# Performance work log

Hardware: AMD Instinct MI355X
Metric: run time of the kernel (lower is better)

Reference implementation:

```python
import jax, jax.numpy as jnp
import numpy as np

T = 16          # video_length
HEADS = 8
DIM_HEAD = 64
INNER = HEADS * DIM_HEAD   # 512
SCALE = DIM_HEAD ** -0.5
QDIM = 320      # input_dims[0]
NTOK = 1024     # num_tokens[0] == N == M (pose tokens)
CTOK = 256      # context_tokens == per-frame context tokens (16x16)
HC = WC = 16    # sqrt(CTOK)
HM = WM = 32    # after bilinear x2 upsample (sqrt(NTOK))
CDIM = 1024     # context_dim
NBLOCKS = 2
FF_INNER = 4 * QDIM  # 1280, GEGLU proj -> 2*FF_INNER


def _ln(x, w, b):
    mu = jnp.mean(x, axis=-1, keepdims=True)
    var = jnp.mean(jnp.square(x - mu), axis=-1, keepdims=True)
    return (x - mu) * jax.lax.rsqrt(var + 1e-5) * w + b


def setup_inputs() -> dict:
    key = jax.random.key(0)
    ks = jax.random.split(key, 24)
    rn = lambda i, shape, s: jax.random.normal(ks[i], shape, jnp.float32) * s
    return {
        "hidden_state": rn(0, (2 * T, NTOK, HEADS, QDIM // HEADS), 1.0),
        "context": rn(1, (2, 2, CTOK, CDIM), 1.0),
        "pose": rn(2, (2, QDIM, T, HM, WM), 1.0),
        "Wq": rn(3, (NBLOCKS, QDIM, INNER), 0.02),
        "Wk": rn(4, (NBLOCKS, CDIM, INNER), 0.02),
        "Wv": rn(5, (NBLOCKS, CDIM, INNER), 0.02),
        "Wa": rn(6, (NBLOCKS, QDIM, INNER), 0.02),
        "agent_bias": rn(7, (NBLOCKS, NTOK, CTOK), 0.01),
        "query_bias": rn(8, (NBLOCKS, NTOK, NTOK), 0.01),
        "dwc_w": rn(9, (NBLOCKS, INNER, 1, 3, 3), 0.1),
        "dwc_b": rn(10, (NBLOCKS, INNER), 0.01),
        "Wo": rn(11, (NBLOCKS, INNER, QDIM), 0.02),
        "norm_w": jnp.ones((QDIM,), jnp.float32),
        "norm_b": jnp.zeros((QDIM,), jnp.float32),
        "ffln_w": jnp.ones((QDIM,), jnp.float32),
        "ffln_b": jnp.zeros((QDIM,), jnp.float32),
        "ff_w1": rn(12, (QDIM, 2 * FF_INNER), 0.02),
        "ff_b1": jnp.zeros((2 * FF_INNER,), jnp.float32),
        "ff_w2": rn(13, (FF_INNER, QDIM), 0.02),
        "ff_b2": jnp.zeros((QDIM,), jnp.float32),
    }


def reference(hidden_state, context, pose, Wq, Wk, Wv, Wa, agent_bias, query_bias,
              dwc_w, dwc_b, Wo, norm_w, norm_b, ffln_w, ffln_b, ff_w1, ff_b1, ff_w2, ff_b2):
    B = hidden_state.shape[0] // T
    C = context.shape[1]
    # '(B T) N H D -> B T N (H D)'
    hs = hidden_state.reshape(B, T, NTOK, QDIM)
    # pose 'B D T H W -> B T (H W) D'
    pose_t = jnp.transpose(pose, (0, 2, 3, 4, 1)).reshape(B, T, NTOK, QDIM)

    for b in range(NBLOCKS):
        # ---- compute_kv_attention ----
        k = jnp.einsum('bcnd,de->bcne', context, Wk[b])          # [B,C,Nc,INNER]
        v = jnp.einsum('bcnd,de->bcne', context, Wv[b])          # [B,C,Nc,INNER]
        a_tok = jnp.einsum('btmd,de->btme', pose_t, Wa[b])       # [B,T,M,INNER]
        kf = k.reshape(B, C * CTOK, INNER)                       # 'B C N D -> B (C N) D'
        attn = jnp.einsum('btme,bne->btmn', a_tok * SCALE, kf)   # [B,T,M,C*Nc]
        # faithful to torch: view(B,T,M,N,C) then 'B T M N C -> (B C) T M N'
        attn = attn.reshape(B, T, NTOK, CTOK, C).transpose(0, 4, 1, 2, 3)  # [B,C,T,M,Nc]
        attn = jax.nn.softmax(attn + agent_bias[b], axis=-1)
        akv = jnp.einsum('bctmn,bcne->bctme', attn, v)           # [B,C,T,M,INNER]
        agent_kv = jnp.max(akv, axis=1)                          # [B,T,M,INNER]

        # depthwise conv over context-frame value maps (T-independent since v repeated over T)
        v_img = v.transpose(0, 1, 3, 2).reshape(B * C, INNER, HC, WC)
        vd = jax.lax.conv_general_dilated(
            v_img, dwc_w[b], (1, 1), 'SAME', feature_group_count=INNER,
            dimension_numbers=('NCHW', 'OIHW', 'NCHW')) + dwc_b[b][None, :, None, None]
        vd = vd.reshape(B, C, INNER, HC, WC).max(axis=1)         # max over frames
        vd = jax.image.resize(vd, (B, INNER, HM, WM), method='bilinear')  # x2, align_corners=False
        v_tok = vd.reshape(B, INNER, NTOK).transpose(0, 2, 1)[:, None]    # [B,1,N,INNER]

        # ---- agent-token cross attention ----
        nh = _ln(hs, norm_w, norm_b)
        q = jnp.einsum('btnd,de->btne', nh, Wq[b])
        aq = jax.nn.softmax(
            jnp.einsum('btne,btme->btnm', q * SCALE, a_tok) + query_bias[b], axis=-1)
        x = jnp.einsum('btnm,btme->btne', aq, agent_kv) + v_tok
        hs = jnp.einsum('btne,ed->btnd', x, Wo[b]) + hs          # residual

    # ---- LayerNorm + GEGLU FeedForward + residual ----
    h = _ln(hs, ffln_w, ffln_b)
    p = h @ ff_w1 + ff_b1
    a, g = jnp.split(p, 2, axis=-1)
    hs = (a * jax.nn.gelu(g, approximate=False)) @ ff_w2 + ff_b2 + hs
    return hs.reshape(B * T, NTOK, QDIM)
```

## Files before the change

kernel.cpp:

```cpp
#include <hip/hip_runtime.h>
#include <hip/hip_bf16.h>
#include <math.h>

typedef __hip_bfloat16 bf16;
typedef short short8 __attribute__((ext_vector_type(8)));
typedef float floatx4 __attribute__((ext_vector_type(4)));

static const int B2   = 2;
static const int TT   = 16;
static const int NTK  = 1024;
static const int CTK  = 256;
static const int QD   = 320;
static const int INNR = 512;
static const int CD   = 1024;
#define SCALE_ 0.125f

__device__ __forceinline__ ushort f2bu(float x){
  bf16 h = __float2bfloat16(x);
  return *reinterpret_cast<ushort*>(&h);
}


template<int NV>
struct StBf {
  const ushort* src; int ld; int tid;
  short8 r[NV];
  __device__ __forceinline__ void load(int k0){
#pragma unroll
    for(int v=0;v<NV;v++){
      int idx=tid+v*256, rr=idx>>2, kq=idx&3;
      r[v] = *(const short8*)&src[(size_t)rr*ld + k0 + kq*8];
    }
  }
  __device__ __forceinline__ void store(ushort* dst){
#pragma unroll
    for(int v=0;v<NV;v++){
      int idx=tid+v*256, rr=idx>>2, kq=idx&3;
      *(short8*)&dst[rr*32 + ((kq+(rr>>1))&3)*8] = r[v];
    }
  }
};

struct StT128 {
  const float* src; int ld; int tid;
  float4 r[4];
  __device__ __forceinline__ void load(int k0){
#pragma unroll
    for(int i=0;i<4;i++){
      int f4=tid+i*256, rr=f4>>3, kq=f4&7;
      r[i] = *(const float4*)(src + (size_t)rr*ld + k0 + kq*4);
    }
  }
  __device__ __forceinline__ void store(ushort* dst){
#pragma unroll
    for(int i=0;i<4;i++){
      int f4=tid+i*256, rr=f4>>3, kq=f4&7;
      int s=((kq>>1)+(rr>>1))&3;
      float4 v=r[i];
      ushort4 u={f2bu(v.x),f2bu(v.y),f2bu(v.z),f2bu(v.w)};
      *(ushort4*)&dst[rr*32 + s*8 + (kq&1)*4]=u;
    }
  }
};

struct StAtok {
  const float* base; int tid;
  float r[16];
  __device__ __forceinline__ void load(int k0){
#pragma unroll
    for(int i=0;i<16;i++){
      int e=tid+i*256, m=e&127, kk=e>>7;
      r[i]=base[(size_t)(k0+kk)*(TT*NTK) + m];
    }
  }
  __device__ __forceinline__ void store(ushort* dst){
#pragma unroll
    for(int i=0;i<16;i++){
      int e=tid+i*256, m=e&127, kk=e>>7;
      int s=((kk>>3)+(m>>1))&3;
      dst[m*32 + s*8 + (kk&7)]=f2bu(r[i]);
    }
  }
};

template<int NT>
__device__ __forceinline__ void mfma_tiles(const ushort* As, const ushort* Bs,
    floatx4 (&acc)[4][NT], int mOff, int nOff, int lane15, int quad){
  short8 af[4], bfm[NT];
  #pragma unroll
  for(int i=0;i<4;i++){
    int ar = mOff + i*16 + lane15;
    af[i] = *(const short8*)&As[ar*32 + ((quad + (ar>>1))&3)*8];
  }
  #pragma unroll
  for(int j=0;j<NT;j++){
    int br = nOff + j*16 + lane15;
    bfm[j] = *(const short8*)&Bs[br*32 + ((quad + (br>>1))&3)*8];
  }
  #pragma unroll
  for(int i=0;i<4;i++)
    #pragma unroll
    for(int j=0;j<NT;j++)
      acc[i][j] = __builtin_amdgcn_mfma_f32_16x16x32_bf16(af[i], bfm[j], acc[i][j], 0, 0, 0);
}

template<int NT>
__device__ __forceinline__ void zero_acc(floatx4 (&acc)[4][NT]){
  floatx4 z = {0.f,0.f,0.f,0.f};
  #pragma unroll
  for(int i=0;i<4;i++)
    #pragma unroll
    for(int j=0;j<NT;j++) acc[i][j]=z;
}

template<int NT, class SA, class SB>
__device__ __forceinline__ void core_db(SA& sa, SB& sb, int K,
    ushort* As0, ushort* As1, ushort* Bs0, ushort* Bs1,
    floatx4 (&acc)[4][NT], int mOff, int nOff, int lane15, int quad){
  sa.load(0); sb.load(0);
  sa.store(As0); sb.store(Bs0);
  const int nk = K>>5;
  for(int i=0;i<nk-1;i++){
    sa.load((i+1)<<5); sb.load((i+1)<<5);
    __syncthreads();
    mfma_tiles<NT>((i&1)?As1:As0, (i&1)?Bs1:Bs0, acc, mOff,nOff,lane15,quad);
    sa.store((i&1)?As0:As1); sb.store((i&1)?Bs0:Bs1);
  }
  __syncthreads();
  mfma_tiles<NT>(((nk-1)&1)?As1:As0, ((nk-1)&1)?Bs1:Bs0, acc, mOff,nOff,lane15,quad);
}

#define GEMM_IDS(NT_) \
  const int tid=threadIdx.x, w=tid>>6, lane15=tid&15, quad=(tid>>4)&3; \
  const int mOff=(w&1)*64, nOff=(w>>1)*(NT_*16);
#define EPI(NT_) \
  _Pragma("unroll") for(int i=0;i<4;i++) \
  _Pragma("unroll") for(int j=0;j<NT_;j++) \
  _Pragma("unroll") for(int r=0;r<4;r++)
#define ROWG (mOff + i*16 + quad*4 + r)
#define COLG (nOff + j*16 + lane15)

__global__ void __launch_bounds__(256) k_wtrans(const float* __restrict__ W, ushort* __restrict__ WT,
                                                int K, int N){
  __shared__ float t[64][65];
  const int kB = blockIdx.y*64, nB = blockIdx.x*64;
  for(int e=threadIdx.x; e<4096; e+=256){
    int r=e>>6, c=e&63;
    t[r][c] = W[(size_t)(kB+r)*N + nB+c];
  }
  __syncthreads();
  for(int e=threadIdx.x; e<4096; e+=256){
    int r=e>>6, c=e&63;
    WT[(size_t)(nB+r)*K + kB+c] = f2bu(t[c][r]);
  }
}

__global__ void k_ln(const float* __restrict__ hs, const float* __restrict__ w,
                     const float* __restrict__ b, ushort* __restrict__ out, int row0){
  const int r = blockIdx.x, lane = threadIdx.x;
  const float* hr = hs + (size_t)(row0+r)*QD;
  float s=0.f, s2=0.f;
  #pragma unroll
  for(int j=0;j<5;j++){ float v=hr[j*64+lane]; s+=v; s2+=v*v; }
  #pragma unroll
  for(int o=32;o;o>>=1){ s+=__shfl_down(s,o); s2+=__shfl_down(s2,o); }
  s = __shfl(s,0); s2 = __shfl(s2,0);
  float mu=s*(1.f/320.f);
  float var=s2*(1.f/320.f)-mu*mu;
  float rs=rsqrtf(var+1e-5f);
  #pragma unroll
  for(int j=0;j<5;j++){
    int c=j*64+lane;
    out[(size_t)r*QD + c] = f2bu((hr[c]-mu)*rs*w[c]+b[c]);
  }
}

__global__ void __launch_bounds__(256) g_kv(const float* __restrict__ A,
                                            const ushort* __restrict__ wkT, const ushort* __restrict__ wvT,
                                            ushort* __restrict__ kbf, float* __restrict__ vb,
                                            ushort* __restrict__ vbT){
  __shared__ ushort As[2][128*32], Bs[2][128*32];
  GEMM_IDS(4)
  const int z=blockIdx.z, b=z>>1, isv=z&1;
  const ushort* BT = (isv ? wvT : wkT) + (size_t)b*524288;
  const int rB=blockIdx.y*128, cB=blockIdx.x*128;
  floatx4 acc[4][4]; zero_acc<4>(acc);
  StT128 sa{A + (size_t)rB*CD, CD, tid};
  StBf<2> sb{BT + (size_t)cB*CD, CD, tid};
  core_db<4>(sa, sb, CD, As[0],As[1],Bs[0],Bs[1], acc, mOff,nOff,lane15,quad);
  if(!isv){
    ushort* kb = kbf + (size_t)b*524288;
    EPI(4){ kb[(size_t)(rB+ROWG)*INNR + cB+COLG] = f2bu(acc[i][j][r]); }
  }else{
    float* vf = vb + (size_t)b*524288;
    ushort* vT = vbT + (size_t)b*524288;
    EPI(4){
      int row=rB+ROWG, col=cB+COLG;
      float v=acc[i][j][r];
      vf[(size_t)row*INNR + col] = v;
      vT[((size_t)(row>>8)*INNR + col)*CTK + (row&255)] = f2bu(v);
    }
  }
}

__global__ void __launch_bounds__(256) g_atok(const float* __restrict__ pose, const ushort* __restrict__ WaT,
                                              ushort* __restrict__ atok, int pt0){
  __shared__ ushort As[2][128*32], Bs[2][128*32];
  GEMM_IDS(4)
  const int z=blockIdx.z, pt=pt0+z, bb=pt>>4, t=pt&15;
  const int rB=blockIdx.y*128, cB=blockIdx.x*128;
  floatx4 acc[4][4]; zero_acc<4>(acc);
  StAtok sa{pose + ((size_t)(bb*QD)*TT + t)*NTK + rB, tid};
  StBf<2> sb{WaT + (size_t)cB*QD, QD, tid};
  core_db<4>(sa, sb, QD, As[0],As[1],Bs[0],Bs[1], acc, mOff,nOff,lane15,quad);
  EPI(4){ atok[((size_t)z*NTK + rB+ROWG)*INNR + cB+COLG] = f2bu(acc[i][j][r]); }
}

__global__ void __launch_bounds__(256) g_logits(const ushort* __restrict__ atok, const ushort* __restrict__ kbf,
                                                const float* __restrict__ abias, float* __restrict__ lgC, int pt0){
  __shared__ ushort As[2][128*32], Bs[2][128*32];
  GEMM_IDS(4)
  const int z=blockIdx.z, zp=z>>1, c=z&1, pt=pt0+zp, bb=pt>>4;
  const int rB=blockIdx.y*128, cB=blockIdx.x*128;
  floatx4 acc[4][4]; zero_acc<4>(acc);
  StBf<2> sa{atok + ((size_t)zp*NTK + rB)*INNR, INNR, tid};
  StBf<2> sb{kbf + (size_t)(bb*512 + 2*cB + c)*INNR, 2*INNR, tid};
  core_db<4>(sa, sb, INNR, As[0],As[1],Bs[0],Bs[1], acc, mOff,nOff,lane15,quad);
  float* Cz = lgC + (size_t)(zp*2+c)*NTK*CTK;
  EPI(4){
    int row=rB+ROWG, col=cB+COLG;
    Cz[(size_t)row*CTK + col] = acc[i][j][r]*SCALE_ + abias[(size_t)row*CTK + col];
  }
}

__global__ void __launch_bounds__(256) g_pvmax(const ushort* __restrict__ lg_us, const ushort* __restrict__ vT,
                                               ushort* __restrict__ akvT, int pt0){
  __shared__ ushort As[2][128*32], Bs[2][128*32];
  GEMM_IDS(4)
  const int zp=blockIdx.z, pt=pt0+zp, bb=pt>>4;
  const int rB=blockIdx.y*128, cB=blockIdx.x*128;
  floatx4 best[4][4]; zero_acc<4>(best);
  floatx4 acc[4][4];
  for(int c=0;c<2;c++){
    if(c) __syncthreads();
    zero_acc<4>(acc);
    StBf<2> sa{lg_us + ((size_t)(zp*2+c)*NTK + rB)*INNR, INNR, tid};
    StBf<2> sb{vT + ((size_t)(bb*2+c)*INNR + cB)*CTK, CTK, tid};
    core_db<4>(sa, sb, CTK, As[0],As[1],Bs[0],Bs[1], acc, mOff,nOff,lane15,quad);
    if(c==0){
      #pragma unroll
      for(int i=0;i<4;i++)
        #pragma unroll
        for(int j=0;j<4;j++) best[i][j]=acc[i][j];
    }else{
      EPI(4){ best[i][j][r] = fmaxf(best[i][j][r], acc[i][j][r]); }
    }
  }
  #pragma unroll
  for(int i=0;i<4;i++)
    #pragma unroll
    for(int j=0;j<4;j++){
      int col = cB + nOff + j*16 + lane15;
      int row0 = rB + mOff + i*16 + quad*4;
      ushort4 u = { f2bu(best[i][j][0]), f2bu(best[i][j][1]), f2bu(best[i][j][2]), f2bu(best[i][j][3]) };
      *(ushort4*)&akvT[((size_t)zp*INNR + col)*NTK + row0] = u;
    }
}

__global__ void __launch_bounds__(256) g_q(const ushort* __restrict__ lnh, const ushort* __restrict__ WqT,
                                           ushort* __restrict__ qb){
  __shared__ ushort As[2][128*32], Bs[2][128*32];
  GEMM_IDS(4)
  const int rB=blockIdx.y*128, cB=blockIdx.x*128;
  floatx4 acc[4][4]; zero_acc<4>(acc);
  StBf<2> sa{lnh + (size_t)rB*QD, QD, tid};
  StBf<2> sb{WqT + (size_t)cB*QD, QD, tid};
  core_db<4>(sa, sb, QD, As[0],As[1],Bs[0],Bs[1], acc, mOff,nOff,lane15,quad);
  EPI(4){ qb[(size_t)(rB+ROWG)*INNR + cB+COLG] = f2bu(acc[i][j][r]); }
}

__global__ void __launch_bounds__(256) g_aql(const ushort* __restrict__ qb, const ushort* __restrict__ atok,
                                             const float* __restrict__ qbias, float* __restrict__ D){
  __shared__ ushort As[2][128*32], Bs[2][128*32];
  GEMM_IDS(4)
  const int z=blockIdx.z;
  const int rB=blockIdx.y*128, cB=blockIdx.x*128;
  floatx4 acc[4][4]; zero_acc<4>(acc);
  StBf<2> sa{qb + ((size_t)z*NTK + rB)*INNR, INNR, tid};
  StBf<2> sb{atok + ((size_t)z*NTK + cB)*INNR, INNR, tid};
  core_db<4>(sa, sb, INNR, As[0],As[1],Bs[0],Bs[1], acc, mOff,nOff,lane15,quad);
  float* Dz = D + (size_t)z*NTK*NTK;
  EPI(4){
    int row=rB+ROWG, col=cB+COLG;
    Dz[(size_t)row*NTK + col] = acc[i][j][r]*SCALE_ + qbias[(size_t)row*NTK + col];
  }
}

__global__ void __launch_bounds__(256) g_aqpv(const float* __restrict__ D, const ushort* __restrict__ akvT,
                                              const float* __restrict__ vt, ushort* __restrict__ xb, int pt0){
  __shared__ ushort As[2][128*32], Bs[2][128*32];
  GEMM_IDS(4)
  const int z=blockIdx.z, pt=pt0+z, bb=pt>>4;
  const int rB=blockIdx.y*128, cB=blockIdx.x*128;
  floatx4 acc[4][4]; zero_acc<4>(acc);
  StBf<2> sa{(const ushort*)D + (size_t)z*2097152 + (size_t)rB*2048, 2048, tid};
  StBf<2> sb{akvT + ((size_t)z*INNR + cB)*NTK, NTK, tid};
  core_db<4>(sa, sb, NTK, As[0],As[1],Bs[0],Bs[1], acc, mOff,nOff,lane15,quad);
  EPI(4){
    int row=rB+ROWG, col=cB+COLG;
    xb[((size_t)z*NTK + row)*INNR + col] = f2bu(acc[i][j][r] + vt[((size_t)bb*NTK + row)*INNR + col]);
  }
}

__global__ void __launch_bounds__(256) g_wo(const ushort* __restrict__ xb, const ushort* __restrict__ WoT,
                                            float* __restrict__ hs, int row0){
  __shared__ ushort As[2][128*32], Bs[2][64*32];
  GEMM_IDS(2)
  const int rB=blockIdx.y*128, cB=blockIdx.x*64;
  floatx4 acc[4][2]; zero_acc<2>(acc);
  StBf<2> sa{xb + (size_t)rB*INNR, INNR, tid};
  StBf<1> sb{WoT + (size_t)cB*INNR, INNR, tid};
  core_db<2>(sa, sb, INNR, As[0],As[1],Bs[0],Bs[1], acc, mOff,nOff,lane15,quad);
  EPI(2){
    size_t o = (size_t)(row0+rB+ROWG)*QD + cB+COLG;
    hs[o] = hs[o] + acc[i][j][r];
  }
}

__global__ void __launch_bounds__(256) g_ff1(const ushort* __restrict__ lnh, const ushort* __restrict__ W1T,
    const float* __restrict__ b1, ushort* __restrict__ G){
  __shared__ ushort As[2][128*32], Ba[2][64*32], Bg[2][64*32];
  GEMM_IDS(2)
  const int rB=blockIdx.y*128, cB=blockIdx.x*64;
  floatx4 accA[4][2], accG[4][2]; zero_acc<2>(accA); zero_acc<2>(accG);
  StBf<2> sa{lnh + (size_t)rB*QD, QD, tid};
  StBf<1> s1{W1T + (size_t)cB*QD, QD, tid};
  StBf<1> s2{W1T + (size_t)(1280+cB)*QD, QD, tid};
  sa.load(0); s1.load(0); s2.load(0);
  sa.store(As[0]); s1.store(Ba[0]); s2.store(Bg[0]);
  const int nk = QD>>5;
  for(int i=0;i<nk-1;i++){
    int k=(i+1)<<5;
    sa.load(k); s1.load(k); s2.load(k);
    __syncthreads();
    const int cur=i&1;
    mfma_tiles<2>(As[cur],Ba[cur],accA,mOff,nOff,lane15,quad);
    mfma_tiles<2>(As[cur],Bg[cur],accG,mOff,nOff,lane15,quad);
    sa.store(As[cur^1]); s1.store(Ba[cur^1]); s2.store(Bg[cur^1]);
  }
  __syncthreads();
  {
    const int cur=(nk-1)&1;
    mfma_tiles<2>(As[cur],Ba[cur],accA,mOff,nOff,lane15,quad);
    mfma_tiles<2>(As[cur],Bg[cur],accG,mOff,nOff,lane15,quad);
  }
  EPI(2){
    int n = cB+COLG;
    float a = accA[i][j][r] + b1[n];
    float g = accG[i][j][r] + b1[1280+n];
    G[(size_t)(rB+ROWG)*1280 + n] = f2bu(a*0.5f*g*(1.0f+erff(g*0.70710678f)));
  }
}

__global__ void __launch_bounds__(256) g_ff2(const ushort* __restrict__ G, const ushort* __restrict__ W2T,
    const float* __restrict__ b2v, float* __restrict__ hs, int row0){
  __shared__ ushort As[2][128*32], Bs[2][64*32];
  GEMM_IDS(2)
  const int rB=blockIdx.y*128, cB=blockIdx.x*64;
  floatx4 acc[4][2]; zero_acc<2>(acc);
  StBf<2> sa{G + (size_t)rB*1280, 1280, tid};
  StBf<1> sb{W2T + (size_t)cB*1280, 1280, tid};
  core_db<2>(sa, sb, 1280, As[0],As[1],Bs[0],Bs[1], acc, mOff,nOff,lane15,quad);
  EPI(2){
    int col = cB+COLG;
    size_t o = (size_t)(row0+rB+ROWG)*QD + col;
    hs[o] = acc[i][j][r] + b2v[col] + hs[o];
  }
}

__global__ void k_softmax256(float* __restrict__ buf){
  __shared__ float red[8];
  const int tid=threadIdx.x;
  size_t row=blockIdx.x;
  float x = buf[row*256+tid];
  float m = x;
  #pragma unroll
  for(int o=32;o;o>>=1) m=fmaxf(m,__shfl_down(m,o));
  if((tid&63)==0) red[tid>>6]=m;
  __syncthreads();
  if(tid==0) red[4]=fmaxf(fmaxf(red[0],red[1]),fmaxf(red[2],red[3]));
  __syncthreads();
  float M=red[4];
  float e=__expf(x-M);
  float s=e;
  #pragma unroll
  for(int o=32;o;o>>=1) s+=__shfl_down(s,o);
  if((tid&63)==0) red[tid>>6]=s;
  __syncthreads();
  if(tid==0) red[5]=red[0]+red[1]+red[2]+red[3];
  __syncthreads();
  ((ushort*)buf)[row*512 + tid] = f2bu(e/red[5]);
}

__global__ void k_softmax1024(float* __restrict__ buf){
  __shared__ float red[8];
  const int tid=threadIdx.x;
  size_t row=blockIdx.x;
  float4* p = (float4*)(buf + row*1024);
  float4 v = p[tid];
  float m = fmaxf(fmaxf(v.x,v.y),fmaxf(v.z,v.w));
  #pragma unroll
  for(int o=32;o;o>>=1) m=fmaxf(m,__shfl_down(m,o));
  if((tid&63)==0) red[tid>>6]=m;
  __syncthreads();
  if(tid==0) red[4]=fmaxf(fmaxf(red[0],red[1]),fmaxf(red[2],red[3]));
  __syncthreads();
  float M=red[4];
  v.x=__expf(v.x-M); v.y=__expf(v.y-M); v.z=__expf(v.z-M); v.w=__expf(v.w-M);
  float s=v.x+v.y+v.z+v.w;
  #pragma unroll
  for(int o=32;o;o>>=1) s+=__shfl_down(s,o);
  if((tid&63)==0) red[tid>>6]=s;
  __syncthreads();
  if(tid==0) red[5]=red[0]+red[1]+red[2]+red[3];
  __syncthreads();
  float inv=1.0f/red[5];
  ushort4 u = { f2bu(v.x*inv), f2bu(v.y*inv), f2bu(v.z*inv), f2bu(v.w*inv) };
  *(ushort4*)((ushort*)buf + row*2048 + (size_t)tid*4) = u;
}

__global__ void k_conv(const float* __restrict__ vbuf, const float* __restrict__ w3,
                       const float* __restrict__ wb, float* __restrict__ vm){
  int idx = blockIdx.x*256+threadIdx.x;
  if(idx >= B2*CTK*INNR) return;
  int e = idx & 511, hw = (idx>>9)&255, b = idx>>17;
  int h = hw>>4, w = hw&15;
  float wt[9];
  #pragma unroll
  for(int q=0;q<9;q++) wt[q]=w3[e*9+q];
  float bias = wb[e];
  float best=0.f;
  for(int c=0;c<2;c++){
    float s = bias;
    #pragma unroll
    for(int dy=-1;dy<=1;dy++)
      #pragma unroll
      for(int dx=-1;dx<=1;dx++){
        int hh=h+dy, ww=w+dx;
        if(hh>=0&&hh<16&&ww>=0&&ww<16)
          s += wt[(dy+1)*3+(dx+1)]*vbuf[((size_t)(b*2+c)*CTK + hh*16+ww)*INNR + e];
      }
    best = c ? fmaxf(best,s) : s;
  }
  vm[((size_t)b*CTK + hw)*INNR + e] = best;
}

__device__ __forceinline__ void up_wt(int i, int& j0, int& j1, float& w){
  float s = 0.5f*i - 0.25f;
  float f = floorf(s);
  w = s - f;
  int a = (int)f;
  j0 = min(15, max(0, a));
  j1 = min(15, max(0, a+1));
}
__global__ void k_up(const float* __restrict__ vm, float* __restrict__ vt){
  int idx = blockIdx.x*256+threadIdx.x;
  if(idx >= B2*NTK*INNR) return;
  int e = idx & 511, n = (idx>>9)&1023, b = idx>>19;
  int hm = n>>5, wm = n&31;
  int h0,h1,w0,w1; float fh,fw;
  up_wt(hm,h0,h1,fh); up_wt(wm,w0,w1,fw);
  const float* base = vm + (size_t)b*CTK*INNR + e;
  float v00=base[(size_t)(h0*16+w0)*INNR], v01=base[(size_t)(h0*16+w1)*INNR];
  float v10=base[(size_t)(h1*16+w0)*INNR], v11=base[(size_t)(h1*16+w1)*INNR];
  vt[((size_t)b*NTK+n)*INNR+e] = (1.f-fh)*((1.f-fw)*v00+fw*v01) + fh*((1.f-fw)*v10+fw*v11);
}


extern "C" void kernel_launch(void* const* d_in, const int* in_sizes, int n_in,
                              void* d_out, int out_size, void* d_ws, size_t ws_size,
                              hipStream_t stream){
  const float* hidden = (const float*)d_in[0];
  const float* context= (const float*)d_in[1];
  const float* pose   = (const float*)d_in[2];
  const float* Wq  = (const float*)d_in[3];
  const float* Wk  = (const float*)d_in[4];
  const float* Wv  = (const float*)d_in[5];
  const float* Wa  = (const float*)d_in[6];
  const float* abias=(const float*)d_in[7];
  const float* qbias=(const float*)d_in[8];
  const float* dwcw=(const float*)d_in[9];
  const float* dwcb=(const float*)d_in[10];
  const float* Wo  = (const float*)d_in[11];
  const float* nw  = (const float*)d_in[12];
  const float* nb  = (const float*)d_in[13];
  const float* fw  = (const float*)d_in[14];
  const float* fb  = (const float*)d_in[15];
  const float* W1  = (const float*)d_in[16];
  const float* b1  = (const float*)d_in[17];
  const float* W2  = (const float*)d_in[18];
  const float* b2v = (const float*)d_in[19];

  float* ws = (float*)d_ws;
  const size_t wsfl = ws_size / 4;

  int S;
  {
    const size_t need16 = 6610944ull + 16ull*2260992ull;
    S = (wsfl >= need16) ? 16 : 4;
  }
  const int NCH = 32 / S;

  size_t off = 0;
  auto take = [&](size_t n){ size_t o = off; off += n; return o; };
  float*  vm   = ws + take(262144);
  float*  vb   = ws + take(1048576);
  float*  vt   = ws + take(2097152);
  ushort* kbf  = (ushort*)(ws + take(524288));
  ushort* vbT  = (ushort*)(ws + take(524288));
  ushort* lnh  = (ushort*)(ws + take((size_t)S*163840));
  ushort* wkT  = (ushort*)(ws + take(524288));
  ushort* wvT  = (ushort*)(ws + take(524288));
  ushort* wqT  = (ushort*)(ws + take(163840));
  ushort* waT  = (ushort*)(ws + take(163840));
  ushort* woT  = (ushort*)(ws + take(163840));
  ushort* w1T  = (ushort*)(ws + take(409600));
  ushort* w2T  = (ushort*)(ws + take(204800));
  float*  SH   = ws + take((size_t)S*1048576);
  ushort* atok = (ushort*)(ws + take((size_t)S*262144));
  ushort* akvT = (ushort*)(ws + take((size_t)S*262144));
  ushort* qbf  = (ushort*)(ws + take((size_t)S*262144));
  ushort* xbf  = (ushort*)(ws + take((size_t)S*262144));

  float* hs = (float*)d_out;

  hipMemcpyAsync(hs, hidden, (size_t)B2*TT*NTK*QD*sizeof(float),
                 hipMemcpyDeviceToDevice, stream);

  for(int b=0;b<2;b++){
    k_wtrans<<<dim3(8,16),256,0,stream>>>(Wk+(size_t)b*CD*INNR,  wkT+(size_t)b*524288, CD, INNR);
    k_wtrans<<<dim3(8,16),256,0,stream>>>(Wv+(size_t)b*CD*INNR,  wvT+(size_t)b*524288, CD, INNR);
    k_wtrans<<<dim3(8,5), 256,0,stream>>>(Wq+(size_t)b*QD*INNR,  wqT+(size_t)b*163840, QD, INNR);
    k_wtrans<<<dim3(8,5), 256,0,stream>>>(Wa+(size_t)b*QD*INNR,  waT+(size_t)b*163840, QD, INNR);
    k_wtrans<<<dim3(5,8), 256,0,stream>>>(Wo+(size_t)b*INNR*QD,  woT+(size_t)b*163840, INNR, QD);
  }
  k_wtrans<<<dim3(40,5),256,0,stream>>>(W1, w1T, QD, 2560);
  k_wtrans<<<dim3(5,20),256,0,stream>>>(W2, w2T, 1280, QD);

  g_kv<<<dim3(4,8,4),256,0,stream>>>(context, wkT, wvT, kbf, vb, vbT);
  for(int b=0;b<2;b++){
    k_conv<<<(B2*CTK*INNR)/256,256,0,stream>>>(vb + (size_t)b*524288,
        dwcw+(size_t)b*INNR*9, dwcb+(size_t)b*INNR, vm);
    k_up<<<(B2*NTK*INNR)/256,256,0,stream>>>(vm, vt + (size_t)b*1048576);
  }

  for(int b=0;b<2;b++){
    const ushort* kbf_b = kbf + (size_t)b*524288;
    const ushort* vbT_b = vbT + (size_t)b*524288;
    const float*  vt_b  = vt  + (size_t)b*1048576;
    for(int ch=0; ch<NCH; ch++){
      const int pt0 = ch*S;
      g_atok<<<dim3(4,8,S),256,0,stream>>>(pose, waT+(size_t)b*163840, atok, pt0);
      g_logits<<<dim3(2,8,2*S),256,0,stream>>>(atok, kbf_b, abias+(size_t)b*NTK*CTK, SH, pt0);
      k_softmax256<<<2*S*1024,256,0,stream>>>(SH);
      g_pvmax<<<dim3(4,8,S),256,0,stream>>>((const ushort*)SH, vbT_b, akvT, pt0);
      k_ln<<<S*1024,64,0,stream>>>(hs, nw, nb, lnh, pt0*1024);
      g_q<<<dim3(4,S*8),256,0,stream>>>(lnh, wqT+(size_t)b*163840, qbf);
      g_aql<<<dim3(8,8,S),256,0,stream>>>(qbf, atok, qbias+(size_t)b*NTK*NTK, SH);
      k_softmax1024<<<S*1024,256,0,stream>>>(SH);
      g_aqpv<<<dim3(4,8,S),256,0,stream>>>(SH, akvT, vt_b, xbf, pt0);
      g_wo<<<dim3(5,S*8),256,0,stream>>>(xbf, woT+(size_t)b*163840, hs, pt0*1024);
    }
  }

  for(int ch=0; ch<NCH; ch++){
    const int row0 = ch*S*1024;
    k_ln<<<S*1024,64,0,stream>>>(hs, fw, fb, lnh, row0);
    g_ff1<<<dim3(20,S*8),256,0,stream>>>(lnh, w1T, b1, (ushort*)SH);
    g_ff2<<<dim3(5,S*8),256,0,stream>>>((ushort*)SH, w2T, b2v, hs, row0);
  }
}
```

Measured before the change: 1.315 ms.

## Deepen GEMM prefetch to two K-tiles ahead using paired register stagers

Restructures the shared GEMM main loop so each K step holds two register staging sets, loading tile k+2 and k+3 while tiles k and k+1 are computed from the LDS double buffer. The goal is to hide more global-load latency behind MFMA work in every projection, attention and FFN GEMM. It doubles staging registers per thread, which may lower occupancy, and assumes every K is a multiple of 64 (all K values here are).

```diff
diff --git a/kernel.cpp b/kernel.cpp
--- a/kernel.cpp
+++ b/kernel.cpp
@@ -114,20 +114,23 @@
 }
 
 template<int NT, class SA, class SB>
-__device__ __forceinline__ void core_db(SA& sa, SB& sb, int K,
+__device__ __forceinline__ void core_db(SA& sa0, SA& sa1, SB& sb0, SB& sb1, int K,
     ushort* As0, ushort* As1, ushort* Bs0, ushort* Bs1,
     floatx4 (&acc)[4][NT], int mOff, int nOff, int lane15, int quad){
-  sa.load(0); sb.load(0);
-  sa.store(As0); sb.store(Bs0);
   const int nk = K>>5;
-  for(int i=0;i<nk-1;i++){
-    sa.load((i+1)<<5); sb.load((i+1)<<5);
+  sa0.load(0);  sb0.load(0);
+  sa1.load(32); sb1.load(32);
+  sa0.store(As0); sb0.store(Bs0);
+  for(int i=0;i<nk;i+=2){
+    if(i+2<nk){ sa0.load((i+2)<<5); sb0.load((i+2)<<5); }
     __syncthreads();
-    mfma_tiles<NT>((i&1)?As1:As0, (i&1)?Bs1:Bs0, acc, mOff,nOff,lane15,quad);
-    sa.store((i&1)?As0:As1); sb.store((i&1)?Bs0:Bs1);
-  }
-  __syncthreads();
-  mfma_tiles<NT>(((nk-1)&1)?As1:As0, ((nk-1)&1)?Bs1:Bs0, acc, mOff,nOff,lane15,quad);
+    mfma_tiles<NT>(As0,Bs0,acc,mOff,nOff,lane15,quad);
+    sa1.store(As1); sb1.store(Bs1);
+    if(i+3<nk){ sa1.load((i+3)<<5); sb1.load((i+3)<<5); }
+    __syncthreads();
+    mfma_tiles<NT>(As1,Bs1,acc,mOff,nOff,lane15,quad);
+    if(i+2<nk){ sa0.store(As0); sb0.store(Bs0); }
+  }
 }
 
 #define GEMM_IDS(NT_) \
@@ -185,9 +188,9 @@
   const ushort* BT = (isv ? wvT : wkT) + (size_t)b*524288;
   const int rB=blockIdx.y*128, cB=blockIdx.x*128;
   floatx4 acc[4][4]; zero_acc<4>(acc);
-  StT128 sa{A + (size_t)rB*CD, CD, tid};
-  StBf<2> sb{BT + (size_t)cB*CD, CD, tid};
-  core_db<4>(sa, sb, CD, As[0],As[1],Bs[0],Bs[1], acc, mOff,nOff,lane15,quad);
+  StT128 sa0{A + (size_t)rB*CD, CD, tid}, sa1{A + (size_t)rB*CD, CD, tid};
+  StBf<2> sb0{BT + (size_t)cB*CD, CD, tid}, sb1{BT + (size_t)cB*CD, CD, tid};
+  core_db<4>(sa0, sa1, sb0, sb1, CD, As[0],As[1],Bs[0],Bs[1], acc, mOff,nOff,lane15,quad);
   if(!isv){
     ushort* kb = kbf + (size_t)b*524288;
     EPI(4){ kb[(size_t)(rB+ROWG)*INNR + cB+COLG] = f2bu(acc[i][j][r]); }
@@ -210,9 +213,10 @@
   const int z=blockIdx.z, pt=pt0+z, bb=pt>>4, t=pt&15;
   const int rB=blockIdx.y*128, cB=blockIdx.x*128;
   floatx4 acc[4][4]; zero_acc<4>(acc);
-  StAtok sa{pose + ((size_t)(bb*QD)*TT + t)*NTK + rB, tid};
-  StBf<2> sb{WaT + (size_t)cB*QD, QD, tid};
-  core_db<4>(sa, sb, QD, As[0],As[1],Bs[0],Bs[1], acc, mOff,nOff,lane15,quad);
+  const float* pbase = pose + ((size_t)(bb*QD)*TT + t)*NTK + rB;
+  StAtok sa0{pbase, tid}, sa1{pbase, tid};
+  StBf<2> sb0{WaT + (size_t)cB*QD, QD, tid}, sb1{WaT + (size_t)cB*QD, QD, tid};
+  core_db<4>(sa0, sa1, sb0, sb1, QD, As[0],As[1],Bs[0],Bs[1], acc, mOff,nOff,lane15,quad);
   EPI(4){ atok[((size_t)z*NTK + rB+ROWG)*INNR + cB+COLG] = f2bu(acc[i][j][r]); }
 }
 
@@ -223,9 +227,11 @@
   const int z=blockIdx.z, zp=z>>1, c=z&1, pt=pt0+zp, bb=pt>>4;
   const int rB=blockIdx.y*128, cB=blockIdx.x*128;
   floatx4 acc[4][4]; zero_acc<4>(acc);
-  StBf<2> sa{atok + ((size_t)zp*NTK + rB)*INNR, INNR, tid};
-  StBf<2> sb{kbf + (size_t)(bb*512 + 2*cB + c)*INNR, 2*INNR, tid};
-  core_db<4>(sa, sb, INNR, As[0],As[1],Bs[0],Bs[1], acc, mOff,nOff,lane15,quad);
+  const ushort* ap = atok + ((size_t)zp*NTK + rB)*INNR;
+  const ushort* bp = kbf + (size_t)(bb*512 + 2*cB + c)*INNR;
+  StBf<2> sa0{ap, INNR, tid}, sa1{ap, INNR, tid};
+  StBf<2> sb0{bp, 2*INNR, tid}, sb1{bp, 2*INNR, tid};
+  core_db<4>(sa0, sa1, sb0, sb1, INNR, As[0],As[1],Bs[0],Bs[1], acc, mOff,nOff,lane15,quad);
   float* Cz = lgC + (size_t)(zp*2+c)*NTK*CTK;
   EPI(4){
     int row=rB+ROWG, col=cB+COLG;
@@ -244,9 +250,11 @@
   for(int c=0;c<2;c++){
     if(c) __syncthreads();
     zero_acc<4>(acc);
-    StBf<2> sa{lg_us + ((size_t)(zp*2+c)*NTK + rB)*INNR, INNR, tid};
-    StBf<2> sb{vT + ((size_t)(bb*2+c)*INNR + cB)*CTK, CTK, tid};
-    core_db<4>(sa, sb, CTK, As[0],As[1],Bs[0],Bs[1], acc, mOff,nOff,lane15,quad);
+    const ushort* ap = lg_us + ((size_t)(zp*2+c)*NTK + rB)*INNR;
+    const ushort* bp = vT + ((size_t)(bb*2+c)*INNR + cB)*CTK;
+    StBf<2> sa0{ap, INNR, tid}, sa1{ap, INNR, tid};
+    StBf<2> sb0{bp, CTK, tid}, sb1{bp, CTK, tid};
+    core_db<4>(sa0, sa1, sb0, sb1, CTK, As[0],As[1],Bs[0],Bs[1], acc, mOff,nOff,lane15,quad);
     if(c==0){
       #pragma unroll
       for(int i=0;i<4;i++)
@@ -273,9 +281,11 @@
   GEMM_IDS(4)
   const int rB=blockIdx.y*128, cB=blockIdx.x*128;
   floatx4 acc[4][4]; zero_acc<4>(acc);
-  StBf<2> sa{lnh + (size_t)rB*QD, QD, tid};
-  StBf<2> sb{WqT + (size_t)cB*QD, QD, tid};
-  core_db<4>(sa, sb, QD, As[0],As[1],Bs[0],Bs[1], acc, mOff,nOff,lane15,quad);
+  const ushort* ap = lnh + (size_t)rB*QD;
+  const ushort* bp = WqT + (size_t)cB*QD;
+  StBf<2> sa0{ap, QD, tid}, sa1{ap, QD, tid};
+  StBf<2> sb0{bp, QD, tid}, sb1{bp, QD, tid};
+  core_db<4>(sa0, sa1, sb0, sb1, QD, As[0],As[1],Bs[0],Bs[1], acc, mOff,nOff,lane15,quad);
   EPI(4){ qb[(size_t)(rB+ROWG)*INNR + cB+COLG] = f2bu(acc[i][j][r]); }
 }
 
@@ -286,9 +296,11 @@
   const int z=blockIdx.z;
   const int rB=blockIdx.y*128, cB=blockIdx.x*128;
   floatx4 acc[4][4]; zero_acc<4>(acc);
-  StBf<2> sa{qb + ((size_t)z*NTK + rB)*INNR, INNR, tid};
-  StBf<2> sb{atok + ((size_t)z*NTK + cB)*INNR, INNR, tid};
-  core_db<4>(sa, sb, INNR, As[0],As[1],Bs[0],Bs[1], acc, mOff,nOff,lane15,quad);
+  const ushort* ap = qb + ((size_t)z*NTK + rB)*INNR;
+  const ushort* bp = atok + ((size_t)z*NTK + cB)*INNR;
+  StBf<2> sa0{ap, INNR, tid}, sa1{ap, INNR, tid};
+  StBf<2> sb0{bp, INNR, tid}, sb1{bp, INNR, tid};
+  core_db<4>(sa0, sa1, sb0, sb1, INNR, As[0],As[1],Bs[0],Bs[1], acc, mOff,nOff,lane15,quad);
   float* Dz = D + (size_t)z*NTK*NTK;
   EPI(4){
     int row=rB+ROWG, col=cB+COLG;
@@ -303,9 +315,11 @@
   const int z=blockIdx.z, pt=pt0+z, bb=pt>>4;
   const int rB=blockIdx.y*128, cB=blockIdx.x*128;
   floatx4 acc[4][4]; zero_acc<4>(acc);
-  StBf<2> sa{(const ushort*)D + (size_t)z*2097152 + (size_t)rB*2048, 2048, tid};
-  StBf<2> sb{akvT + ((size_t)z*INNR + cB)*NTK, NTK, tid};
-  core_db<4>(sa, sb, NTK, As[0],As[1],Bs[0],Bs[1], acc, mOff,nOff,lane15,quad);
+  const ushort* ap = (const ushort*)D + (size_t)z*2097152 + (size_t)rB*2048;
+  const ushort* bp = akvT + ((size_t)z*INNR + cB)*NTK;
+  StBf<2> sa0{ap, 2048, tid}, sa1{ap, 2048, tid};
+  StBf<2> sb0{bp, NTK, tid}, sb1{bp, NTK, tid};
+  core_db<4>(sa0, sa1, sb0, sb1, NTK, As[0],As[1],Bs[0],Bs[1], acc, mOff,nOff,lane15,quad);
   EPI(4){
     int row=rB+ROWG, col=cB+COLG;
     xb[((size_t)z*NTK + row)*INNR + col] = f2bu(acc[i][j][r] + vt[((size_t)bb*NTK + row)*INNR + col]);
@@ -318,9 +332,11 @@
   GEMM_IDS(2)
   const int rB=blockIdx.y*128, cB=blockIdx.x*64;
   floatx4 acc[4][2]; zero_acc<2>(acc);
-  StBf<2> sa{xb + (size_t)rB*INNR, INNR, tid};
-  StBf<1> sb{WoT + (size_t)cB*INNR, INNR, tid};
-  core_db<2>(sa, sb, INNR, As[0],As[1],Bs[0],Bs[1], acc, mOff,nOff,lane15,quad);
+  const ushort* ap = xb + (size_t)rB*INNR;
+  const ushort* bp = WoT + (size_t)cB*INNR;
+  StBf<2> sa0{ap, INNR, tid}, sa1{ap, INNR, tid};
+  StBf<1> sb0{bp, INNR, tid}, sb1{bp, INNR, tid};
+  core_db<2>(sa0, sa1, sb0, sb1, INNR, As[0],As[1],Bs[0],Bs[1], acc, mOff,nOff,lane15,quad);
   EPI(2){
     size_t o = (size_t)(row0+rB+ROWG)*QD + cB+COLG;
     hs[o] = hs[o] + acc[i][j][r];
@@ -333,26 +349,27 @@
   GEMM_IDS(2)
   const int rB=blockIdx.y*128, cB=blockIdx.x*64;
   floatx4 accA[4][2], accG[4][2]; zero_acc<2>(accA); zero_acc<2>(accG);
-  StBf<2> sa{lnh + (size_t)rB*QD, QD, tid};
-  StBf<1> s1{W1T + (size_t)cB*QD, QD, tid};
-  StBf<1> s2{W1T + (size_t)(1280+cB)*QD, QD, tid};
-  sa.load(0); s1.load(0); s2.load(0);
-  sa.store(As[0]); s1.store(Ba[0]); s2.store(Bg[0]);
+  const ushort* ap = lnh + (size_t)rB*QD;
+  const ushort* p1 = W1T + (size_t)cB*QD;
+  const ushort* p2 = W1T + (size_t)(1280+cB)*QD;
+  StBf<2> sa0{ap, QD, tid}, sa1{ap, QD, tid};
+  StBf<1> s10{p1, QD, tid}, s11{p1, QD, tid};
+  StBf<1> s20{p2, QD, tid}, s21{p2, QD, tid};
   const int nk = QD>>5;
-  for(int i=0;i<nk-1;i++){
-    int k=(i+1)<<5;
-    sa.load(k); s1.load(k); s2.load(k);
+  sa0.load(0);  s10.load(0);  s20.load(0);
+  sa1.load(32); s11.load(32); s21.load(32);
+  sa0.store(As[0]); s10.store(Ba[0]); s20.store(Bg[0]);
+  for(int i=0;i<nk;i+=2){
+    if(i+2<nk){ sa0.load((i+2)<<5); s10.load((i+2)<<5); s20.load((i+2)<<5); }
     __syncthreads();
-    const int cur=i&1;
-    mfma_tiles<2>(As[cur],Ba[cur],accA,mOff,nOff,lane15,quad);
-    mfma_tiles<2>(As[cur],Bg[cur],accG,mOff,nOff,lane15,quad);
-    sa.store(As[cur^1]); s1.store(Ba[cur^1]); s2.store(Bg[cur^1]);
-  }
-  __syncthreads();
-  {
-    const int cur=(nk-1)&1;
-    mfma_tiles<2>(As[cur],Ba[cur],accA,mOff,nOff,lane15,quad);
-    mfma_tiles<2>(As[cur],Bg[cur],accG,mOff,nOff,lane15,quad);
+    mfma_tiles<2>(As[0],Ba[0],accA,mOff,nOff,lane15,quad);
+    mfma_tiles<2>(As[0],Bg[0],accG,mOff,nOff,lane15,quad);
+    sa1.store(As[1]); s11.store(Ba[1]); s21.store(Bg[1]);
+    if(i+3<nk){ sa1.load((i+3)<<5); s11.load((i+3)<<5); s21.load((i+3)<<5); }
+    __syncthreads();
+    mfma_tiles<2>(As[1],Ba[1],accA,mOff,nOff,lane15,quad);
+    mfma_tiles<2>(As[1],Bg[1],accG,mOff,nOff,lane15,quad);
+    if(i+2<nk){ sa0.store(As[0]); s10.store(Ba[0]); s20.store(Bg[0]); }
   }
   EPI(2){
     int n = cB+COLG;
@@ -368,9 +385,11 @@
   GEMM_IDS(2)
   const int rB=blockIdx.y*128, cB=blockIdx.x*64;
   floatx4 acc[4][2]; zero_acc<2>(acc);
-  StBf<2> sa{G + (size_t)rB*1280, 1280, tid};
-  StBf<1> sb{W2T + (size_t)cB*1280, 1280, tid};
-  core_db<2>(sa, sb, 1280, As[0],As[1],Bs[0],Bs[1], acc, mOff,nOff,lane15,quad);
+  const ushort* ap = G + (size_t)rB*1280;
+  const ushort* bp = W2T + (size_t)cB*1280;
+  StBf<2> sa0{ap, 1280, tid}, sa1{ap, 1280, tid};
+  StBf<1> sb0{bp, 1280, tid}, sb1{bp, 1280, tid};
+  core_db<2>(sa0, sa1, sb0, sb1, 1280, As[0],As[1],Bs[0],Bs[1], acc, mOff,nOff,lane15,quad);
   EPI(2){
     int col = cB+COLG;
     size_t o = (size_t)(row0+rB+ROWG)*QD + col;
```

Result: slower. 1.404 ms (+6.8%).
